# Performance work log

Measured on AMD Instinct MI355X. Metric: run time of the kernel, lower is better.

The kernel has to match this reference:

```python
import jax, jax.numpy as jnp
import numpy as np

N_NODES = 100000
N_EDGES = 1600000
IN_CH, HID_CH, OUT_CH = 128, 64, 32


def setup_inputs() -> dict:
    key = jax.random.key(0)
    k = jax.random.split(key, 8)
    x = jax.random.normal(k[0], (N_NODES, IN_CH), dtype=jnp.float32)
    edge_index = jax.random.randint(k[1], (2, N_EDGES), 0, N_NODES, dtype=jnp.int32)
    edge_weight = jax.random.uniform(k[2], (N_EDGES,), dtype=jnp.float32)
    # Glorot-ish init for GCNConv linear weights, zero bias (torch default bias init is uniform; zeros is fine for a reference)
    W1 = jax.random.normal(k[3], (IN_CH, HID_CH), dtype=jnp.float32) * (1.0 / np.sqrt(IN_CH))
    b1 = jnp.zeros((HID_CH,), dtype=jnp.float32)
    W2 = jax.random.normal(k[4], (HID_CH, OUT_CH), dtype=jnp.float32) * (1.0 / np.sqrt(HID_CH))
    b2 = jnp.zeros((OUT_CH,), dtype=jnp.float32)
    return {"x": x, "edge_index": edge_index, "edge_weight": edge_weight,
            "W1": W1, "b1": b1, "W2": W2, "b2": b2}


def _gcn_norm(edge_index, edge_weight, num_nodes):
    # add self-loops with weight 1 (GCNConv default, add_self_loops=True)
    loop = jnp.arange(num_nodes, dtype=edge_index.dtype)
    src = jnp.concatenate([edge_index[0], loop])
    dst = jnp.concatenate([edge_index[1], loop])
    w = jnp.concatenate([edge_weight, jnp.ones((num_nodes,), edge_weight.dtype)])
    deg = jax.ops.segment_sum(w, dst, num_segments=num_nodes)  # [N]
    dinv = jnp.where(deg > 0, jax.lax.rsqrt(deg), 0.0)
    norm = dinv[src] * w * dinv[dst]  # [E+N]
    return src, dst, norm


def _gcn_conv(x, W, b, src, dst, norm, num_nodes):
    h = x @ W                                  # [N, C_out] dense GEMM
    msg = h[src] * norm[:, None]               # gather + scale, [E+N, C_out]
    agg = jax.ops.segment_sum(msg, dst, num_segments=num_nodes)  # scatter-add
    return agg + b


def reference(x, edge_index, edge_weight, W1, b1, W2, b2):
    n = x.shape[0]
    src, dst, norm = _gcn_norm(edge_index, edge_weight, n)
    # dropout is identity in eval mode
    h = _gcn_conv(x, W1, b1, src, dst, norm, n)
    h = jax.nn.relu(h)
    h = jax.nn.leaky_relu(h)  # identity on non-negative input, kept for faithfulness
    out = _gcn_conv(h, W2, b2, src, dst, norm, n)
    return out
```

## Files before the change

### kernel.cpp

```cpp
#include <hip/hip_runtime.h>
#include <hip/hip_bf16.h>


constexpr int CAP    = 48;
constexpr int SHIFT  = 7;
constexpr int BNODES = 128;
constexpr int NBLK   = 128;

__device__ __forceinline__ unsigned short f2bf_rne(float f) {
    unsigned u = __float_as_uint(f);
    unsigned r = (u + 0x7FFFu + ((u >> 16) & 1u)) >> 16;
    return (unsigned short)r;
}

__device__ __forceinline__ void bf8_fma(uint4 u, float s, float* acc) {
    acc[0] = fmaf(__uint_as_float(u.x << 16),          s, acc[0]);
    acc[1] = fmaf(__uint_as_float(u.x & 0xffff0000u),  s, acc[1]);
    acc[2] = fmaf(__uint_as_float(u.y << 16),          s, acc[2]);
    acc[3] = fmaf(__uint_as_float(u.y & 0xffff0000u),  s, acc[3]);
    acc[4] = fmaf(__uint_as_float(u.z << 16),          s, acc[4]);
    acc[5] = fmaf(__uint_as_float(u.z & 0xffff0000u),  s, acc[5]);
    acc[6] = fmaf(__uint_as_float(u.w << 16),          s, acc[6]);
    acc[7] = fmaf(__uint_as_float(u.w & 0xffff0000u),  s, acc[7]);
}

__global__ __launch_bounds__(256) void k_ph1(const int* __restrict__ dst,
                                             unsigned* __restrict__ hmat,
                                             int E, int NB, int chunk) {
    __shared__ unsigned hist[1024];
    const int tid = threadIdx.x;
    for (int j = tid; j < NB; j += 256) hist[j] = 0;
    __syncthreads();
    const int lo = blockIdx.x * chunk;
    const int hi = min(lo + chunk, E);
    for (int e = lo + tid; e < hi; e += 256)
        atomicAdd(&hist[dst[e] >> SHIFT], 1u);
    __syncthreads();
    for (int j = tid; j < NB; j += 256)
        hmat[(size_t)blockIdx.x * NB + j] = hist[j];
}

__global__ __launch_bounds__(256) void k_ph2a(unsigned* __restrict__ hmat,
                                              unsigned* __restrict__ colsum, int NB) {
    const int lane = threadIdx.x & 63;
    const int j = blockIdx.x * 4 + (threadIdx.x >> 6);
    if (j >= NB) return;
    unsigned v0 = hmat[(size_t)(2 * lane) * NB + j];
    unsigned v1 = hmat[(size_t)(2 * lane + 1) * NB + j];
    unsigned s = v0 + v1;
    unsigned inc = s;
    #pragma unroll
    for (int off = 1; off < 64; off <<= 1) {
        unsigned u = __shfl_up(inc, off, 64);
        if (lane >= off) inc += u;
    }
    unsigned excl = inc - s;
    hmat[(size_t)(2 * lane) * NB + j] = excl;
    hmat[(size_t)(2 * lane + 1) * NB + j] = excl + v0;
    if (lane == 63) colsum[j] = inc;
}

__global__ __launch_bounds__(1024) void k_ph2b(const unsigned* __restrict__ colsum,
                                               unsigned* __restrict__ bucketbase, int NB) {
    __shared__ unsigned wtot[16];
    const int t = threadIdx.x;
    const int lane = t & 63, wv = t >> 6;
    unsigned v = (t < NB) ? colsum[t] : 0;
    unsigned inc = v;
    #pragma unroll
    for (int off = 1; off < 64; off <<= 1) {
        unsigned u = __shfl_up(inc, off, 64);
        if (lane >= off) inc += u;
    }
    if (lane == 63) wtot[wv] = inc;
    __syncthreads();
    unsigned wbase = 0;
    for (int w = 0; w < wv; ++w) wbase += wtot[w];
    if (t < NB) bucketbase[t] = wbase + inc - v;
}

__global__ __launch_bounds__(256) void k_pscatter(const int* __restrict__ src,
                                                  const int* __restrict__ dst,
                                                  const float* __restrict__ w,
                                                  const unsigned* __restrict__ hmat,
                                                  const unsigned* __restrict__ bucketbase,
                                                  unsigned long long* __restrict__ ebuf,
                                                  int E, int NB, int chunk) {
    __shared__ unsigned cur[1024];
    const int tid = threadIdx.x;
    for (int j = tid; j < NB; j += 256)
        cur[j] = bucketbase[j] + hmat[(size_t)blockIdx.x * NB + j];
    __syncthreads();
    const int lo = blockIdx.x * chunk;
    const int hi = min(lo + chunk, E);
    for (int e = lo + tid; e < hi; e += 256) {
        const int d = dst[e];
        const int b = d >> SHIFT;
        unsigned pos = atomicAdd(&cur[b], 1u);
        unsigned long long word =
            ((unsigned long long)__float_as_uint(w[e]) << 32) |
            ((unsigned)src[e] << SHIFT) | (unsigned)(d & (BNODES - 1));
        ebuf[pos] = word;
    }
}

__global__ __launch_bounds__(256) void k_build2(const unsigned long long* __restrict__ ebuf,
                                                const unsigned* __restrict__ bucketbase,
                                                const unsigned* __restrict__ colsum,
                                                unsigned* __restrict__ slots,
                                                int2* __restrict__ meta, int n, int NB) {
    __shared__ unsigned cnt[BNODES];
    __shared__ float wsum[BNODES];
    const int j = blockIdx.x;
    const int tid = threadIdx.x;
    if (tid < BNODES) { cnt[tid] = 0; wsum[tid] = 0.f; }
    __syncthreads();
    const unsigned base = bucketbase[j];
    const int m = (int)colsum[j];
    for (int t = tid; t < m; t += 256) {
        unsigned long long word = ebuf[base + t];
        unsigned lo32 = (unsigned)word;
        int dl = lo32 & (BNODES - 1);
        int s  = (int)(lo32 >> SHIFT);
        float wv = __uint_as_float((unsigned)(word >> 32));
        int k = atomicAdd(&cnt[dl], 1u);
        atomicAdd(&wsum[dl], wv);
        if (k < CAP) {
            unsigned wq = (unsigned)(wv * 32767.f + 0.5f);
            slots[((size_t)(j << SHIFT) + dl) * CAP + k] = ((unsigned)s << 15) | wq;
        }
    }
    __syncthreads();
    if (tid < BNODES) {
        int node = (j << SHIFT) + tid;
        if (node < n) {
            int c = min((int)cnt[tid], CAP);
            float dv = rsqrtf(1.f + wsum[tid]);
            meta[node] = make_int2(c, __float_as_int(dv));
        }
    }
}

__global__ __launch_bounds__(256) void k_gemm1(const float* __restrict__ x,
                                               const float* __restrict__ W,
                                               const int2* __restrict__ meta,
                                               unsigned short* __restrict__ h, int n) {
    constexpr int TM = 64, BK = 16;
    __shared__ float xs[BK][TM + 4];
    __shared__ float ws[BK][64 + 4];
    const int tid = threadIdx.x;
    const int tx = tid & 15, ty = tid >> 4;
    const int r0 = blockIdx.x * TM;

    float acc[4][4] = {};
    for (int k0 = 0; k0 < 128; k0 += BK) {
        {
            int kk = tid & 15;
            int row = tid >> 4;
            #pragma unroll
            for (int p = 0; p < 4; ++p) {
                int rr = row + p * 16;
                xs[kk][rr] = (r0 + rr < n) ? x[(size_t)(r0 + rr) * 128 + k0 + kk] : 0.f;
            }
        }
        {
            int c = tid & 63;
            int kb = tid >> 6;
            #pragma unroll
            for (int p = 0; p < 4; ++p) {
                int kk = kb + p * 4;
                ws[kk][c] = W[(size_t)(k0 + kk) * 64 + c];
            }
        }
        __syncthreads();
        #pragma unroll
        for (int kk = 0; kk < BK; ++kk) {
            const float4 av = *reinterpret_cast<const float4*>(&xs[kk][ty * 4]);
            const float4 bv = *reinterpret_cast<const float4*>(&ws[kk][tx * 4]);
            const float a[4] = {av.x, av.y, av.z, av.w};
            const float b[4] = {bv.x, bv.y, bv.z, bv.w};
            #pragma unroll
            for (int i = 0; i < 4; ++i)
                #pragma unroll
                for (int j = 0; j < 4; ++j)
                    acc[i][j] = fmaf(a[i], b[j], acc[i][j]);
        }
        __syncthreads();
    }
    #pragma unroll
    for (int i = 0; i < 4; ++i) {
        int r = r0 + ty * 4 + i;
        if (r < n) {
            const float sc = __int_as_float(meta[r].y);
            ushort4 o;
            o.x = f2bf_rne(acc[i][0] * sc);
            o.y = f2bf_rne(acc[i][1] * sc);
            o.z = f2bf_rne(acc[i][2] * sc);
            o.w = f2bf_rne(acc[i][3] * sc);
            *reinterpret_cast<ushort4*>(&h[(size_t)r * 64 + tx * 4]) = o;
        }
    }
}

__global__ __launch_bounds__(256) void k_layer1(const unsigned short* __restrict__ h1,
                                                const unsigned* __restrict__ slots,
                                                const int2* __restrict__ meta,
                                                const float* __restrict__ b1,
                                                const float* __restrict__ W2,
                                                unsigned short* __restrict__ h2, int n) {
    const int lane = threadIdx.x & 63;
    const int wid = (blockIdx.x * blockDim.x + threadIdx.x) >> 6;
    const int nwaves = (gridDim.x * blockDim.x) >> 6;
    const int g = lane >> 3;
    const int q = lane & 7;
    const int half = lane >> 5, c = lane & 31;

    float w[32];
    #pragma unroll
    for (int m = 0; m < 32; ++m)
        w[m] = W2[(half * 32 + m) * 32 + c];
    float bb[8];
    #pragma unroll
    for (int m = 0; m < 8; ++m) bb[m] = b1[q * 8 + m];
    const float selfw = (g == 0) ? 1.0f : 0.f;

    int v = wid;
    int2 mt = make_int2(0, 0);
    unsigned pa0 = 0, pb0 = 0;
    if (v < n) {
        mt = meta[v];
        const unsigned* pk = slots + (size_t)v * CAP;
        pa0 = pk[g];
        pb0 = pk[8 + g];
    }
    for (; v < n; v += nwaves) {
        const int vn = v + nwaves;
        int2 mtn = make_int2(0, 0);
        if (vn < n) mtn = meta[vn];

        const float di = __int_as_float(mt.y);
        const int cnt = mt.x;
        const unsigned* pk = slots + (size_t)v * CAP;

        float acc[8] = {0.f, 0.f, 0.f, 0.f, 0.f, 0.f, 0.f, 0.f};
        bf8_fma(*reinterpret_cast<const uint4*>(&h1[(size_t)v * 64 + q * 8]), selfw, acc);

        const int rounds = (cnt + 15) >> 4;
        unsigned pa = pa0, pb = pb0;
        for (int r = 0; r < rounds; ++r) {
            const int base = r << 4;
            unsigned na = pa, nb = pb;
            if (r + 1 < rounds) { na = pk[base + 16 + g]; nb = pk[base + 24 + g]; }
            const int ea = base + g, eb = base + 8 + g;
            const int   ia = (ea < cnt) ? (int)(pa >> 15) : v;
            const float wa = (ea < cnt) ? (float)(pa & 0x7fffu) * (1.0f / 32767.f) : 0.f;
            const int   ib = (eb < cnt) ? (int)(pb >> 15) : v;
            const float wb = (eb < cnt) ? (float)(pb & 0x7fffu) * (1.0f / 32767.f) : 0.f;
            uint4 ua = *reinterpret_cast<const uint4*>(&h1[(size_t)ia * 64 + q * 8]);
            uint4 ub = *reinterpret_cast<const uint4*>(&h1[(size_t)ib * 64 + q * 8]);
            bf8_fma(ua, wa, acc);
            bf8_fma(ub, wb, acc);
            pa = na; pb = nb;
        }
        {
            const unsigned* pkn = slots + (size_t)(vn < n ? vn : 0) * CAP;
            pa0 = pkn[g];
            pb0 = pkn[8 + g];
        }

        #pragma unroll
        for (int m = 0; m < 8; ++m) {
            acc[m] += __shfl_xor(acc[m], 8, 64);
            acc[m] += __shfl_xor(acc[m], 16, 64);
            acc[m] += __shfl_xor(acc[m], 32, 64);
        }

        float r8[8];
        #pragma unroll
        for (int m = 0; m < 8; ++m) r8[m] = fmaxf(fmaf(acc[m], di, bb[m]), 0.f);

        float o = 0.f;
        #pragma unroll
        for (int m = 0; m < 32; ++m) {
            float rv = __shfl(r8[m & 7], half * 4 + (m >> 3), 64);
            o = fmaf(rv, w[m], o);
        }
        o += __shfl_xor(o, 32, 64);
        if (half == 0) h2[(size_t)v * 32 + c] = f2bf_rne(o * di);

        mt = mtn;
    }
}

__global__ __launch_bounds__(256) void k_layer2(const unsigned short* __restrict__ h2,
                                                const unsigned* __restrict__ slots,
                                                const int2* __restrict__ meta,
                                                const float* __restrict__ b2,
                                                float* __restrict__ out, int n) {
    const int lane = threadIdx.x & 63;
    const int wid = (blockIdx.x * blockDim.x + threadIdx.x) >> 6;
    const int nwaves = (gridDim.x * blockDim.x) >> 6;
    const int g = lane >> 2;
    const int q = lane & 3;
    float bb[8];
    #pragma unroll
    for (int m = 0; m < 8; ++m) bb[m] = b2[q * 8 + m];
    const float selfw = (g == 0) ? 1.0f : 0.f;

    int v = wid;
    int2 mt = make_int2(0, 0);
    unsigned pa0 = 0;
    if (v < n) {
        mt = meta[v];
        pa0 = (slots + (size_t)v * CAP)[g];
    }
    for (; v < n; v += nwaves) {
        const int vn = v + nwaves;
        int2 mtn = make_int2(0, 0);
        if (vn < n) mtn = meta[vn];

        const float di = __int_as_float(mt.y);
        const int cnt = mt.x;
        const unsigned* pk = slots + (size_t)v * CAP;

        float acc[8] = {0.f, 0.f, 0.f, 0.f, 0.f, 0.f, 0.f, 0.f};
        bf8_fma(*reinterpret_cast<const uint4*>(&h2[(size_t)v * 32 + q * 8]), selfw, acc);

        const int rounds = (cnt + 15) >> 4;
        unsigned pa = pa0;
        for (int r = 0; r < rounds; ++r) {
            unsigned na = pa;
            if (r + 1 < rounds) na = pk[(r << 4) + 16 + g];
            const int e = (r << 4) + g;
            const int   ia = (e < cnt) ? (int)(pa >> 15) : v;
            const float wa = (e < cnt) ? (float)(pa & 0x7fffu) * (1.0f / 32767.f) : 0.f;
            uint4 ua = *reinterpret_cast<const uint4*>(&h2[(size_t)ia * 32 + q * 8]);
            bf8_fma(ua, wa, acc);
            pa = na;
        }
        pa0 = (slots + (size_t)(vn < n ? vn : 0) * CAP)[g];

        #pragma unroll
        for (int m = 0; m < 8; ++m) {
            acc[m] += __shfl_xor(acc[m], 4, 64);
            acc[m] += __shfl_xor(acc[m], 8, 64);
            acc[m] += __shfl_xor(acc[m], 16, 64);
            acc[m] += __shfl_xor(acc[m], 32, 64);
        }

        if (g == 0) {
            float4 o0 = make_float4(fmaf(acc[0], di, bb[0]), fmaf(acc[1], di, bb[1]),
                                    fmaf(acc[2], di, bb[2]), fmaf(acc[3], di, bb[3]));
            float4 o1 = make_float4(fmaf(acc[4], di, bb[4]), fmaf(acc[5], di, bb[5]),
                                    fmaf(acc[6], di, bb[6]), fmaf(acc[7], di, bb[7]));
            *reinterpret_cast<float4*>(&out[(size_t)v * 32 + q * 8]) = o0;
            *reinterpret_cast<float4*>(&out[(size_t)v * 32 + q * 8 + 4]) = o1;
        }
        mt = mtn;
    }
}

extern "C" void kernel_launch(void* const* d_in, const int* in_sizes, int n_in,
                              void* d_out, int out_size, void* d_ws, size_t ws_size,
                              hipStream_t stream) {
    const float* x  = (const float*)d_in[0];
    const int*   ei = (const int*)d_in[1];
    const float* ew = (const float*)d_in[2];
    const float* W1 = (const float*)d_in[3];
    const float* b1 = (const float*)d_in[4];
    const float* W2 = (const float*)d_in[5];
    const float* b2 = (const float*)d_in[6];
    float* out = (float*)d_out;

    const int n = in_sizes[0] / 128;
    const int E = in_sizes[2];
    const int* src = ei;
    const int* dst = ei + E;

    const int NB = (n + BNODES - 1) >> SHIFT;
    const int chunk = (E + NBLK - 1) / NBLK;

    char* p = (char*)d_ws;
    unsigned* hmat = (unsigned*)p;                            p += (size_t)NBLK * NB * 4;
    unsigned* colsum = (unsigned*)p;                          p += 4096;
    unsigned* bucketbase = (unsigned*)p;                      p += 4096;
    p = (char*)(((uintptr_t)p + 15) & ~(uintptr_t)15);
    unsigned long long* ebuf = (unsigned long long*)p;        p += (size_t)E * 8;
    unsigned* slots = (unsigned*)p;                           p += (size_t)n * CAP * 4;
    int2* meta = (int2*)p;                                    p += (size_t)n * 8;
    unsigned short* h1 = (unsigned short*)p;                  p += (size_t)n * 64 * 2;
    unsigned short* h2 = (unsigned short*)p;

    k_ph1<<<NBLK, 256, 0, stream>>>(dst, hmat, E, NB, chunk);
    k_ph2a<<<(NB + 3) / 4, 256, 0, stream>>>(hmat, colsum, NB);
    k_ph2b<<<1, 1024, 0, stream>>>(colsum, bucketbase, NB);
    k_pscatter<<<NBLK, 256, 0, stream>>>(src, dst, ew, hmat, bucketbase, ebuf, E, NB, chunk);
    k_build2<<<NB, 256, 0, stream>>>(ebuf, bucketbase, colsum, slots, meta, n, NB);

    k_gemm1<<<(n + 63) / 64, 256, 0, stream>>>(x, W1, meta, h1, n);
    k_layer1<<<2048, 256, 0, stream>>>(h1, slots, meta, b1, W2, h2, n);
    k_layer2<<<2048, 256, 0, stream>>>(h2, slots, meta, b2, out, n);
}
```

Measured before the change: 213.9 us.

## Process two nodes per wavefront in GCN aggregation kernels and stage W2 in LDS

Both aggregation kernels now handle a pair of adjacent nodes per wave, interleaving their slot and neighbor-feature gathers to raise memory-level parallelism, and load both nodes' meta with one int4 read. Layer1 moves W2 from 32 per-lane registers into shared memory, freeing registers for the doubled accumulators. The cross-iteration prefetch of the next node's meta and slots is dropped, and each pair runs for the larger of the two neighbor counts, so work is wasted when degrees differ. Workspace buffers are padded by two nodes to allow the out-of-range second node reads.

```diff
diff --git a/kernel.cpp b/kernel.cpp
--- a/kernel.cpp
+++ b/kernel.cpp
@@ -23,6 +23,7 @@
     acc[6] = fmaf(__uint_as_float(u.w << 16),          s, acc[6]);
     acc[7] = fmaf(__uint_as_float(u.w & 0xffff0000u),  s, acc[7]);
 }
+
 
 __global__ __launch_bounds__(256) void k_ph1(const int* __restrict__ dst,
                                              unsigned* __restrict__ hmat,
@@ -208,6 +209,17 @@
                                                 const float* __restrict__ b1,
                                                 const float* __restrict__ W2,
                                                 unsigned short* __restrict__ h2, int n) {
+    __shared__ float wlds[64][32];
+    {
+        const int t = threadIdx.x;
+        #pragma unroll
+        for (int i = 0; i < 8; ++i) {
+            int idx = t + i * 256;
+            wlds[idx >> 5][idx & 31] = W2[idx];
+        }
+    }
+    __syncthreads();
+
     const int lane = threadIdx.x & 63;
     const int wid = (blockIdx.x * blockDim.x + threadIdx.x) >> 6;
     const int nwaves = (gridDim.x * blockDim.x) >> 6;
@@ -215,80 +227,85 @@
     const int q = lane & 7;
     const int half = lane >> 5, c = lane & 31;
 
-    float w[32];
-    #pragma unroll
-    for (int m = 0; m < 32; ++m)
-        w[m] = W2[(half * 32 + m) * 32 + c];
     float bb[8];
     #pragma unroll
     for (int m = 0; m < 8; ++m) bb[m] = b1[q * 8 + m];
     const float selfw = (g == 0) ? 1.0f : 0.f;
 
-    int v = wid;
-    int2 mt = make_int2(0, 0);
-    unsigned pa0 = 0, pb0 = 0;
-    if (v < n) {
-        mt = meta[v];
-        const unsigned* pk = slots + (size_t)v * CAP;
-        pa0 = pk[g];
-        pb0 = pk[8 + g];
-    }
-    for (; v < n; v += nwaves) {
-        const int vn = v + nwaves;
-        int2 mtn = make_int2(0, 0);
-        if (vn < n) mtn = meta[vn];
-
-        const float di = __int_as_float(mt.y);
-        const int cnt = mt.x;
-        const unsigned* pk = slots + (size_t)v * CAP;
-
-        float acc[8] = {0.f, 0.f, 0.f, 0.f, 0.f, 0.f, 0.f, 0.f};
-        bf8_fma(*reinterpret_cast<const uint4*>(&h1[(size_t)v * 64 + q * 8]), selfw, acc);
-
-        const int rounds = (cnt + 15) >> 4;
-        unsigned pa = pa0, pb = pb0;
+    const int npairs = (n + 1) >> 1;
+    for (int i = wid; i < npairs; i += nwaves) {
+        const int v0 = 2 * i, v1 = v0 + 1;
+        const bool has1 = (v1 < n);
+        const int4 mm = *reinterpret_cast<const int4*>(&meta[v0]);
+        const int c0 = mm.x;
+        const int c1 = has1 ? mm.z : 0;
+        const float di0 = __int_as_float(mm.y);
+        const float di1 = __int_as_float(mm.w);
+        const unsigned* pk0 = slots + (size_t)v0 * CAP;
+        const unsigned* pk1 = pk0 + CAP;
+
+        float a0[8] = {0.f, 0.f, 0.f, 0.f, 0.f, 0.f, 0.f, 0.f};
+        float a1[8] = {0.f, 0.f, 0.f, 0.f, 0.f, 0.f, 0.f, 0.f};
+        bf8_fma(*reinterpret_cast<const uint4*>(&h1[(size_t)v0 * 64 + q * 8]), selfw, a0);
+        bf8_fma(*reinterpret_cast<const uint4*>(&h1[(size_t)v1 * 64 + q * 8]), selfw, a1);
+
+        const int rounds = max((c0 + 15) >> 4, (c1 + 15) >> 4);
+        unsigned s0a = pk0[g], s0b = pk0[8 + g];
+        unsigned s1a = pk1[g], s1b = pk1[8 + g];
         for (int r = 0; r < rounds; ++r) {
             const int base = r << 4;
-            unsigned na = pa, nb = pb;
-            if (r + 1 < rounds) { na = pk[base + 16 + g]; nb = pk[base + 24 + g]; }
+            const unsigned t0a = s0a, t0b = s0b, t1a = s1a, t1b = s1b;
+            if (r + 1 < rounds) {
+                s0a = pk0[base + 16 + g]; s0b = pk0[base + 24 + g];
+                s1a = pk1[base + 16 + g]; s1b = pk1[base + 24 + g];
+            }
             const int ea = base + g, eb = base + 8 + g;
-            const int   ia = (ea < cnt) ? (int)(pa >> 15) : v;
-            const float wa = (ea < cnt) ? (float)(pa & 0x7fffu) * (1.0f / 32767.f) : 0.f;
-            const int   ib = (eb < cnt) ? (int)(pb >> 15) : v;
-            const float wb = (eb < cnt) ? (float)(pb & 0x7fffu) * (1.0f / 32767.f) : 0.f;
-            uint4 ua = *reinterpret_cast<const uint4*>(&h1[(size_t)ia * 64 + q * 8]);
-            uint4 ub = *reinterpret_cast<const uint4*>(&h1[(size_t)ib * 64 + q * 8]);
-            bf8_fma(ua, wa, acc);
-            bf8_fma(ub, wb, acc);
-            pa = na; pb = nb;
-        }
-        {
-            const unsigned* pkn = slots + (size_t)(vn < n ? vn : 0) * CAP;
-            pa0 = pkn[g];
-            pb0 = pkn[8 + g];
+            const int   i0a = (ea < c0) ? (int)(t0a >> 15) : v0;
+            const float w0a = (ea < c0) ? (float)(t0a & 0x7fffu) * (1.f / 32767.f) : 0.f;
+            const int   i0b = (eb < c0) ? (int)(t0b >> 15) : v0;
+            const float w0b = (eb < c0) ? (float)(t0b & 0x7fffu) * (1.f / 32767.f) : 0.f;
+            const int   i1a = (ea < c1) ? (int)(t1a >> 15) : v0;
+            const float w1a = (ea < c1) ? (float)(t1a & 0x7fffu) * (1.f / 32767.f) : 0.f;
+            const int   i1b = (eb < c1) ? (int)(t1b >> 15) : v0;
+            const float w1b = (eb < c1) ? (float)(t1b & 0x7fffu) * (1.f / 32767.f) : 0.f;
+            uint4 u0a = *reinterpret_cast<const uint4*>(&h1[(size_t)i0a * 64 + q * 8]);
+            uint4 u0b = *reinterpret_cast<const uint4*>(&h1[(size_t)i0b * 64 + q * 8]);
+            uint4 u1a = *reinterpret_cast<const uint4*>(&h1[(size_t)i1a * 64 + q * 8]);
+            uint4 u1b = *reinterpret_cast<const uint4*>(&h1[(size_t)i1b * 64 + q * 8]);
+            bf8_fma(u0a, w0a, a0);
+            bf8_fma(u0b, w0b, a0);
+            bf8_fma(u1a, w1a, a1);
+            bf8_fma(u1b, w1b, a1);
         }
 
         #pragma unroll
         for (int m = 0; m < 8; ++m) {
-            acc[m] += __shfl_xor(acc[m], 8, 64);
-            acc[m] += __shfl_xor(acc[m], 16, 64);
-            acc[m] += __shfl_xor(acc[m], 32, 64);
-        }
-
-        float r8[8];
-        #pragma unroll
-        for (int m = 0; m < 8; ++m) r8[m] = fmaxf(fmaf(acc[m], di, bb[m]), 0.f);
-
-        float o = 0.f;
+            a0[m] += __shfl_xor(a0[m], 8, 64);  a1[m] += __shfl_xor(a1[m], 8, 64);
+            a0[m] += __shfl_xor(a0[m], 16, 64); a1[m] += __shfl_xor(a1[m], 16, 64);
+            a0[m] += __shfl_xor(a0[m], 32, 64); a1[m] += __shfl_xor(a1[m], 32, 64);
+        }
+
+        float r0_[8], r1_[8];
+        #pragma unroll
+        for (int m = 0; m < 8; ++m) {
+            r0_[m] = fmaxf(fmaf(a0[m], di0, bb[m]), 0.f);
+            r1_[m] = fmaxf(fmaf(a1[m], di1, bb[m]), 0.f);
+        }
+
+        float o0 = 0.f, o1 = 0.f;
         #pragma unroll
         for (int m = 0; m < 32; ++m) {
-            float rv = __shfl(r8[m & 7], half * 4 + (m >> 3), 64);
-            o = fmaf(rv, w[m], o);
-        }
-        o += __shfl_xor(o, 32, 64);
-        if (half == 0) h2[(size_t)v * 32 + c] = f2bf_rne(o * di);
-
-        mt = mtn;
+            const int srcl = half * 4 + (m >> 3);
+            const float wm = wlds[half * 32 + m][c];
+            o0 = fmaf(__shfl(r0_[m & 7], srcl, 64), wm, o0);
+            o1 = fmaf(__shfl(r1_[m & 7], srcl, 64), wm, o1);
+        }
+        o0 += __shfl_xor(o0, 32, 64);
+        o1 += __shfl_xor(o1, 32, 64);
+
+        const float oval = (half == 0) ? o0 * di0 : o1 * di1;
+        if (half == 0 || has1)
+            h2[(size_t)v0 * 32 + lane] = f2bf_rne(oval);
     }
 }
 
@@ -307,56 +324,66 @@
     for (int m = 0; m < 8; ++m) bb[m] = b2[q * 8 + m];
     const float selfw = (g == 0) ? 1.0f : 0.f;
 
-    int v = wid;
-    int2 mt = make_int2(0, 0);
-    unsigned pa0 = 0;
-    if (v < n) {
-        mt = meta[v];
-        pa0 = (slots + (size_t)v * CAP)[g];
-    }
-    for (; v < n; v += nwaves) {
-        const int vn = v + nwaves;
-        int2 mtn = make_int2(0, 0);
-        if (vn < n) mtn = meta[vn];
-
-        const float di = __int_as_float(mt.y);
-        const int cnt = mt.x;
-        const unsigned* pk = slots + (size_t)v * CAP;
-
-        float acc[8] = {0.f, 0.f, 0.f, 0.f, 0.f, 0.f, 0.f, 0.f};
-        bf8_fma(*reinterpret_cast<const uint4*>(&h2[(size_t)v * 32 + q * 8]), selfw, acc);
-
-        const int rounds = (cnt + 15) >> 4;
-        unsigned pa = pa0;
+    const int npairs = (n + 1) >> 1;
+    for (int i = wid; i < npairs; i += nwaves) {
+        const int v0 = 2 * i, v1 = v0 + 1;
+        const bool has1 = (v1 < n);
+        const int4 mm = *reinterpret_cast<const int4*>(&meta[v0]);
+        const int c0 = mm.x;
+        const int c1 = has1 ? mm.z : 0;
+        const float di0 = __int_as_float(mm.y);
+        const float di1 = __int_as_float(mm.w);
+        const unsigned* pk0 = slots + (size_t)v0 * CAP;
+        const unsigned* pk1 = pk0 + CAP;
+
+        float a0[8] = {0.f, 0.f, 0.f, 0.f, 0.f, 0.f, 0.f, 0.f};
+        float a1[8] = {0.f, 0.f, 0.f, 0.f, 0.f, 0.f, 0.f, 0.f};
+        bf8_fma(*reinterpret_cast<const uint4*>(&h2[(size_t)v0 * 32 + q * 8]), selfw, a0);
+        bf8_fma(*reinterpret_cast<const uint4*>(&h2[(size_t)v1 * 32 + q * 8]), selfw, a1);
+
+        const int rounds = max((c0 + 15) >> 4, (c1 + 15) >> 4);
+        unsigned s0 = pk0[g], s1 = pk1[g];
         for (int r = 0; r < rounds; ++r) {
-            unsigned na = pa;
-            if (r + 1 < rounds) na = pk[(r << 4) + 16 + g];
-            const int e = (r << 4) + g;
-            const int   ia = (e < cnt) ? (int)(pa >> 15) : v;
-            const float wa = (e < cnt) ? (float)(pa & 0x7fffu) * (1.0f / 32767.f) : 0.f;
-            uint4 ua = *reinterpret_cast<const uint4*>(&h2[(size_t)ia * 32 + q * 8]);
-            bf8_fma(ua, wa, acc);
-            pa = na;
-        }
-        pa0 = (slots + (size_t)(vn < n ? vn : 0) * CAP)[g];
+            const int base = r << 4;
+            const unsigned t0 = s0, t1 = s1;
+            if (r + 1 < rounds) {
+                s0 = pk0[base + 16 + g];
+                s1 = pk1[base + 16 + g];
+            }
+            const int e = base + g;
+            const int   i0 = (e < c0) ? (int)(t0 >> 15) : v0;
+            const float w0 = (e < c0) ? (float)(t0 & 0x7fffu) * (1.f / 32767.f) : 0.f;
+            const int   i1 = (e < c1) ? (int)(t1 >> 15) : v0;
+            const float w1 = (e < c1) ? (float)(t1 & 0x7fffu) * (1.f / 32767.f) : 0.f;
+            uint4 u0 = *reinterpret_cast<const uint4*>(&h2[(size_t)i0 * 32 + q * 8]);
+            uint4 u1 = *reinterpret_cast<const uint4*>(&h2[(size_t)i1 * 32 + q * 8]);
+            bf8_fma(u0, w0, a0);
+            bf8_fma(u1, w1, a1);
+        }
 
         #pragma unroll
         for (int m = 0; m < 8; ++m) {
-            acc[m] += __shfl_xor(acc[m], 4, 64);
-            acc[m] += __shfl_xor(acc[m], 8, 64);
-            acc[m] += __shfl_xor(acc[m], 16, 64);
-            acc[m] += __shfl_xor(acc[m], 32, 64);
+            a0[m] += __shfl_xor(a0[m], 4, 64);  a1[m] += __shfl_xor(a1[m], 4, 64);
+            a0[m] += __shfl_xor(a0[m], 8, 64);  a1[m] += __shfl_xor(a1[m], 8, 64);
+            a0[m] += __shfl_xor(a0[m], 16, 64); a1[m] += __shfl_xor(a1[m], 16, 64);
+            a0[m] += __shfl_xor(a0[m], 32, 64); a1[m] += __shfl_xor(a1[m], 32, 64);
         }
 
         if (g == 0) {
-            float4 o0 = make_float4(fmaf(acc[0], di, bb[0]), fmaf(acc[1], di, bb[1]),
-                                    fmaf(acc[2], di, bb[2]), fmaf(acc[3], di, bb[3]));
-            float4 o1 = make_float4(fmaf(acc[4], di, bb[4]), fmaf(acc[5], di, bb[5]),
-                                    fmaf(acc[6], di, bb[6]), fmaf(acc[7], di, bb[7]));
-            *reinterpret_cast<float4*>(&out[(size_t)v * 32 + q * 8]) = o0;
-            *reinterpret_cast<float4*>(&out[(size_t)v * 32 + q * 8 + 4]) = o1;
-        }
-        mt = mtn;
+            float4 oA = make_float4(fmaf(a0[0], di0, bb[0]), fmaf(a0[1], di0, bb[1]),
+                                    fmaf(a0[2], di0, bb[2]), fmaf(a0[3], di0, bb[3]));
+            float4 oB = make_float4(fmaf(a0[4], di0, bb[4]), fmaf(a0[5], di0, bb[5]),
+                                    fmaf(a0[6], di0, bb[6]), fmaf(a0[7], di0, bb[7]));
+            *reinterpret_cast<float4*>(&out[(size_t)v0 * 32 + q * 8]) = oA;
+            *reinterpret_cast<float4*>(&out[(size_t)v0 * 32 + q * 8 + 4]) = oB;
+        } else if (g == 1 && has1) {
+            float4 oA = make_float4(fmaf(a1[0], di1, bb[0]), fmaf(a1[1], di1, bb[1]),
+                                    fmaf(a1[2], di1, bb[2]), fmaf(a1[3], di1, bb[3]));
+            float4 oB = make_float4(fmaf(a1[4], di1, bb[4]), fmaf(a1[5], di1, bb[5]),
+                                    fmaf(a1[6], di1, bb[6]), fmaf(a1[7], di1, bb[7]));
+            *reinterpret_cast<float4*>(&out[(size_t)v1 * 32 + q * 8]) = oA;
+            *reinterpret_cast<float4*>(&out[(size_t)v1 * 32 + q * 8 + 4]) = oB;
+        }
     }
 }
 
@@ -386,9 +413,9 @@
     unsigned* bucketbase = (unsigned*)p;                      p += 4096;
     p = (char*)(((uintptr_t)p + 15) & ~(uintptr_t)15);
     unsigned long long* ebuf = (unsigned long long*)p;        p += (size_t)E * 8;
-    unsigned* slots = (unsigned*)p;                           p += (size_t)n * CAP * 4;
-    int2* meta = (int2*)p;                                    p += (size_t)n * 8;
-    unsigned short* h1 = (unsigned short*)p;                  p += (size_t)n * 64 * 2;
+    unsigned* slots = (unsigned*)p;                           p += (size_t)(n + 2) * CAP * 4;
+    int2* meta = (int2*)p;                                    p += (size_t)(n + 2) * 8;
+    unsigned short* h1 = (unsigned short*)p;                  p += (size_t)(n + 2) * 64 * 2;
     unsigned short* h2 = (unsigned short*)p;
 
     k_ph1<<<NBLK, 256, 0, stream>>>(dst, hmat, E, NB, chunk);
```

Result: no change. 216.1 us (+1.0%).

## Process four nodes per wave in layer-2 aggregation with 4-way unrolled gathers

Applied to the files above, without the earlier changes.

The layer-2 aggregation kernel now assigns four destination nodes to each wavefront (16 lanes per node) instead of one node per wave. Each 16-lane group handles one node's edge list with four independent gathers per iteration and prefetches the next slot batch, and the lane reduction shrinks to two shuffles. The aim is to cut wasted lanes on nodes with few edges (about 17 on average) and raise memory-level parallelism. The workspace is padded so the unconditional slot prefetch past CAP and the clamped last node stay in bounds.

```diff
diff --git a/kernel.cpp b/kernel.cpp
--- a/kernel.cpp
+++ b/kernel.cpp
@@ -23,6 +23,7 @@
     acc[6] = fmaf(__uint_as_float(u.w << 16),          s, acc[6]);
     acc[7] = fmaf(__uint_as_float(u.w & 0xffff0000u),  s, acc[7]);
 }
+
 
 __global__ __launch_bounds__(256) void k_ph1(const int* __restrict__ dst,
                                              unsigned* __restrict__ hmat,
@@ -253,9 +254,9 @@
             if (r + 1 < rounds) { na = pk[base + 16 + g]; nb = pk[base + 24 + g]; }
             const int ea = base + g, eb = base + 8 + g;
             const int   ia = (ea < cnt) ? (int)(pa >> 15) : v;
-            const float wa = (ea < cnt) ? (float)(pa & 0x7fffu) * (1.0f / 32767.f) : 0.f;
+            const float wa = (ea < cnt) ? (float)(pa & 0x7fffu) * (1.f / 32767.f) : 0.f;
             const int   ib = (eb < cnt) ? (int)(pb >> 15) : v;
-            const float wb = (eb < cnt) ? (float)(pb & 0x7fffu) * (1.0f / 32767.f) : 0.f;
+            const float wb = (eb < cnt) ? (float)(pb & 0x7fffu) * (1.f / 32767.f) : 0.f;
             uint4 ua = *reinterpret_cast<const uint4*>(&h1[(size_t)ia * 64 + q * 8]);
             uint4 ub = *reinterpret_cast<const uint4*>(&h1[(size_t)ib * 64 + q * 8]);
             bf8_fma(ua, wa, acc);
@@ -300,63 +301,67 @@
     const int lane = threadIdx.x & 63;
     const int wid = (blockIdx.x * blockDim.x + threadIdx.x) >> 6;
     const int nwaves = (gridDim.x * blockDim.x) >> 6;
-    const int g = lane >> 2;
+    const int sub = lane >> 4;
+    const int g = (lane >> 2) & 3;
     const int q = lane & 3;
     float bb[8];
     #pragma unroll
     for (int m = 0; m < 8; ++m) bb[m] = b2[q * 8 + m];
     const float selfw = (g == 0) ? 1.0f : 0.f;
 
-    int v = wid;
-    int2 mt = make_int2(0, 0);
-    unsigned pa0 = 0;
-    if (v < n) {
-        mt = meta[v];
-        pa0 = (slots + (size_t)v * CAP)[g];
-    }
-    for (; v < n; v += nwaves) {
-        const int vn = v + nwaves;
-        int2 mtn = make_int2(0, 0);
-        if (vn < n) mtn = meta[vn];
-
-        const float di = __int_as_float(mt.y);
-        const int cnt = mt.x;
-        const unsigned* pk = slots + (size_t)v * CAP;
+    const int nquads = (n + 3) >> 2;
+    for (int i = wid; i < nquads; i += nwaves) {
+        const int v = 4 * i + sub;
+        const int vc = min(v, n - 1);
+        const int2 mm = meta[vc];
+        const int cnt = (v < n) ? mm.x : 0;
+        const float di = __int_as_float(mm.y);
+        const unsigned* pk = slots + (size_t)vc * CAP;
 
         float acc[8] = {0.f, 0.f, 0.f, 0.f, 0.f, 0.f, 0.f, 0.f};
-        bf8_fma(*reinterpret_cast<const uint4*>(&h2[(size_t)v * 32 + q * 8]), selfw, acc);
-
-        const int rounds = (cnt + 15) >> 4;
-        unsigned pa = pa0;
-        for (int r = 0; r < rounds; ++r) {
-            unsigned na = pa;
-            if (r + 1 < rounds) na = pk[(r << 4) + 16 + g];
-            const int e = (r << 4) + g;
-            const int   ia = (e < cnt) ? (int)(pa >> 15) : v;
-            const float wa = (e < cnt) ? (float)(pa & 0x7fffu) * (1.0f / 32767.f) : 0.f;
-            uint4 ua = *reinterpret_cast<const uint4*>(&h2[(size_t)ia * 32 + q * 8]);
-            bf8_fma(ua, wa, acc);
-            pa = na;
-        }
-        pa0 = (slots + (size_t)(vn < n ? vn : 0) * CAP)[g];
+        bf8_fma(*reinterpret_cast<const uint4*>(&h2[(size_t)vc * 32 + q * 8]), selfw, acc);
+
+        const int rounds = (cnt + 3) >> 2;
+        unsigned s0 = pk[g], s1 = pk[4 + g], s2 = pk[8 + g], s3 = pk[12 + g];
+        for (int r = 0; r < rounds; r += 4) {
+            const unsigned t0 = s0, t1 = s1, t2 = s2, t3 = s3;
+            {
+                const int pb = (r + 4) * 4 + g;
+                s0 = pk[pb]; s1 = pk[pb + 4]; s2 = pk[pb + 8]; s3 = pk[pb + 12];
+            }
+            const int e0 = r * 4 + g, e1 = e0 + 4, e2 = e0 + 8, e3 = e0 + 12;
+            const int   i0 = (e0 < cnt) ? (int)(t0 >> 15) : vc;
+            const float w0 = (e0 < cnt) ? (float)(t0 & 0x7fffu) * (1.f / 32767.f) : 0.f;
+            const int   i1 = (e1 < cnt) ? (int)(t1 >> 15) : vc;
+            const float w1 = (e1 < cnt) ? (float)(t1 & 0x7fffu) * (1.f / 32767.f) : 0.f;
+            const int   i2 = (e2 < cnt) ? (int)(t2 >> 15) : vc;
+            const float w2 = (e2 < cnt) ? (float)(t2 & 0x7fffu) * (1.f / 32767.f) : 0.f;
+            const int   i3 = (e3 < cnt) ? (int)(t3 >> 15) : vc;
+            const float w3 = (e3 < cnt) ? (float)(t3 & 0x7fffu) * (1.f / 32767.f) : 0.f;
+            uint4 u0 = *reinterpret_cast<const uint4*>(&h2[(size_t)i0 * 32 + q * 8]);
+            uint4 u1 = *reinterpret_cast<const uint4*>(&h2[(size_t)i1 * 32 + q * 8]);
+            uint4 u2 = *reinterpret_cast<const uint4*>(&h2[(size_t)i2 * 32 + q * 8]);
+            uint4 u3 = *reinterpret_cast<const uint4*>(&h2[(size_t)i3 * 32 + q * 8]);
+            bf8_fma(u0, w0, acc);
+            bf8_fma(u1, w1, acc);
+            bf8_fma(u2, w2, acc);
+            bf8_fma(u3, w3, acc);
+        }
 
         #pragma unroll
         for (int m = 0; m < 8; ++m) {
             acc[m] += __shfl_xor(acc[m], 4, 64);
             acc[m] += __shfl_xor(acc[m], 8, 64);
-            acc[m] += __shfl_xor(acc[m], 16, 64);
-            acc[m] += __shfl_xor(acc[m], 32, 64);
-        }
-
-        if (g == 0) {
-            float4 o0 = make_float4(fmaf(acc[0], di, bb[0]), fmaf(acc[1], di, bb[1]),
+        }
+
+        if (g == 0 && v < n) {
+            float4 oA = make_float4(fmaf(acc[0], di, bb[0]), fmaf(acc[1], di, bb[1]),
                                     fmaf(acc[2], di, bb[2]), fmaf(acc[3], di, bb[3]));
-            float4 o1 = make_float4(fmaf(acc[4], di, bb[4]), fmaf(acc[5], di, bb[5]),
+            float4 oB = make_float4(fmaf(acc[4], di, bb[4]), fmaf(acc[5], di, bb[5]),
                                     fmaf(acc[6], di, bb[6]), fmaf(acc[7], di, bb[7]));
-            *reinterpret_cast<float4*>(&out[(size_t)v * 32 + q * 8]) = o0;
-            *reinterpret_cast<float4*>(&out[(size_t)v * 32 + q * 8 + 4]) = o1;
-        }
-        mt = mtn;
+            *reinterpret_cast<float4*>(&out[(size_t)v * 32 + q * 8]) = oA;
+            *reinterpret_cast<float4*>(&out[(size_t)v * 32 + q * 8 + 4]) = oB;
+        }
     }
 }
 
@@ -386,9 +391,9 @@
     unsigned* bucketbase = (unsigned*)p;                      p += 4096;
     p = (char*)(((uintptr_t)p + 15) & ~(uintptr_t)15);
     unsigned long long* ebuf = (unsigned long long*)p;        p += (size_t)E * 8;
-    unsigned* slots = (unsigned*)p;                           p += (size_t)n * CAP * 4;
-    int2* meta = (int2*)p;                                    p += (size_t)n * 8;
-    unsigned short* h1 = (unsigned short*)p;                  p += (size_t)n * 64 * 2;
+    unsigned* slots = (unsigned*)p;                           p += ((size_t)(n + 4) * CAP + 64) * 4;
+    int2* meta = (int2*)p;                                    p += (size_t)(n + 4) * 8;
+    unsigned short* h1 = (unsigned short*)p;                  p += (size_t)(n + 4) * 64 * 2;
     unsigned short* h2 = (unsigned short*)p;
 
     k_ph1<<<NBLK, 256, 0, stream>>>(dst, hmat, E, NB, chunk);
```

After: 199.1 us. 6.9% less time.
